# Kernel tuning notes

Hardware: AMD Instinct MI355X
Metric: run time of the kernel (lower is better)

Reference implementation:

```python
import jax, jax.numpy as jnp
import numpy as np

H = 16       # num_heads
D = 64       # head_dim
MBL = 2048   # max_bias_length


def setup_inputs() -> dict:
    key = jax.random.key(0)
    ks = jax.random.split(key, 7)
    B, L, E = 1, 2048, 1024
    s = E ** -0.5  # keep activations O(1)
    return {
        "x": jax.random.normal(ks[0], (B, L, E), jnp.float32),
        "Wq": jax.random.normal(ks[1], (E, E), jnp.float32) * s,
        "Wk": jax.random.normal(ks[2], (E, E), jnp.float32) * s,
        "Wv": jax.random.normal(ks[3], (E, E), jnp.float32) * s,
        "Wo": jax.random.normal(ks[4], (E, E), jnp.float32) * s,
        "bias": jax.random.normal(ks[5], (H, MBL), jnp.float32) * 0.001,
        "tau": jnp.full((H,), -1.0, jnp.float32),
    }


def reference(x, Wq, Wk, Wv, Wo, bias, tau):
    B, L, E = x.shape
    # projections (nn.Linear: y = x @ W.T), split into heads -> [B, H, L, D]
    q = (x @ Wq.T).reshape(B, L, H, D).transpose(0, 2, 1, 3)
    k = (x @ Wk.T).reshape(B, L, H, D).transpose(0, 2, 1, 3)
    v = (x @ Wv.T).reshape(B, L, H, D).transpose(0, 2, 1, 3)

    scale = D ** -0.5
    scores = jnp.einsum("bhqd,bhkd->bhqk", q, k) * scale  # [B,H,L,L]

    pos = jnp.arange(L)
    dist = pos[:, None] - pos[None, :]                     # [L,L] q - k
    dist_clamped = jnp.clip(dist, 0, MBL - 1)
    in_window = (dist >= 0) & (dist < MBL)
    bias_matrix = bias[:, dist_clamped] * in_window.astype(scores.dtype)  # [H,L,L]
    scores = scores + bias_matrix[None]

    causal = dist >= 0
    scores = jnp.where(causal[None, None], scores, -jnp.inf)
    attn = jax.nn.softmax(scores, axis=-1)                 # [B,H,L,L]

    # elastic-softmax correction: relu(attn + tau_h / row_index)
    idx = jnp.arange(1, L + 1, dtype=attn.dtype)           # 1..L per query row
    tau_term = tau[None, :, None, None] / idx[None, None, :, None]
    attn = jax.nn.relu(attn + tau_term)

    out = jnp.einsum("bhqk,bhkd->bhqd", attn, v)           # [B,H,L,D]
    out = out.transpose(0, 2, 1, 3).reshape(B, L, H * D)
    return out @ Wo.T
```

## Files before the change

### kernel.cpp

```cpp
#include <hip/hip_runtime.h>
#include <stdint.h>


typedef unsigned short u16;
typedef __bf16 bf16x8 __attribute__((ext_vector_type(8)));
typedef float f32x4 __attribute__((ext_vector_type(4)));

__device__ __forceinline__ void gl_lds16(const void* g, void* l) {
  __builtin_amdgcn_global_load_lds((const __attribute__((address_space(1))) void*)g,
                                   (__attribute__((address_space(3))) void*)l, 16, 0, 0);
}
__device__ __forceinline__ u16 f2b(float x) {
  return __builtin_bit_cast(u16, (__bf16)x);
}

__global__ __launch_bounds__(256) void conv_all(
    const float* __restrict__ x, const float* __restrict__ wq, const float* __restrict__ wk,
    const float* __restrict__ wv, const float* __restrict__ wo,
    u16* __restrict__ xb, u16* __restrict__ wqb, u16* __restrict__ wkb,
    u16* __restrict__ wvb, u16* __restrict__ wob) {
  int i4 = blockIdx.x * 256 + threadIdx.x;
  const float* s; u16* d; int off;
  if (i4 < 524288)       { s = x;  d = xb;  off = i4; }
  else if (i4 < 786432)  { s = wq; d = wqb; off = i4 - 524288; }
  else if (i4 < 1048576) { s = wk; d = wkb; off = i4 - 786432; }
  else if (i4 < 1310720) { s = wv; d = wvb; off = i4 - 1048576; }
  else                   { s = wo; d = wob; off = i4 - 1310720; }
  float4 v = reinterpret_cast<const float4*>(s)[off];
  ushort4 o;
  o.x = f2b(v.x); o.y = f2b(v.y); o.z = f2b(v.z); o.w = f2b(v.w);
  reinterpret_cast<ushort4*>(d)[off] = o;
}

template <int MT>
__device__ __forceinline__ void gemm_core(const u16* __restrict__ A, const u16* __restrict__ B,
                                          int m0, int n0, u16* As, u16* Bs,
                                          f32x4 (&acc)[MT / 32][4], int w, int l) {
  int lr = l & 15, lg = l >> 4;
  int wr = w >> 1, wc = w & 1;
  for (int k0 = 0; k0 < 1024; k0 += 32) {
    __syncthreads();
#pragma unroll
    for (int j = 0; j < MT / 64; ++j) {
      int flat = j * 256 + w * 64 + l;
      int row = flat >> 2, c = flat & 3;
      int cs = c ^ (row & 3);
      gl_lds16(A + (size_t)(m0 + row) * 1024 + k0 + cs * 8, As + (j * 256 + w * 64) * 8);
    }
#pragma unroll
    for (int j = 0; j < 2; ++j) {
      int flat = j * 256 + w * 64 + l;
      int row = flat >> 2, c = flat & 3;
      int cs = c ^ (row & 3);
      gl_lds16(B + (size_t)(n0 + row) * 1024 + k0 + cs * 8, Bs + (j * 256 + w * 64) * 8);
    }
    __syncthreads();
    bf16x8 af[MT / 32], bfr[4];
#pragma unroll
    for (int mi = 0; mi < MT / 32; ++mi) {
      int row = wr * (MT / 2) + mi * 16 + lr;
      af[mi] = *reinterpret_cast<const bf16x8*>(
          reinterpret_cast<const char*>(As) + row * 64 + ((lg * 16) ^ ((row & 3) << 4)));
    }
#pragma unroll
    for (int ni = 0; ni < 4; ++ni) {
      int row = wc * 64 + ni * 16 + lr;
      bfr[ni] = *reinterpret_cast<const bf16x8*>(
          reinterpret_cast<const char*>(Bs) + row * 64 + ((lg * 16) ^ ((row & 3) << 4)));
    }
#pragma unroll
    for (int mi = 0; mi < MT / 32; ++mi)
#pragma unroll
      for (int ni = 0; ni < 4; ++ni)
        acc[mi][ni] = __builtin_amdgcn_mfma_f32_16x16x32_bf16(af[mi], bfr[ni], acc[mi][ni], 0, 0, 0);
  }
}

__global__ __launch_bounds__(256) void qkv_gemm(
    const u16* __restrict__ xb, const u16* __restrict__ wqb, const u16* __restrict__ wkb,
    const u16* __restrict__ wvb, u16* __restrict__ Qb, u16* __restrict__ Kb, u16* __restrict__ Vtb) {
  __shared__ __align__(16) u16 As[64 * 32];
  __shared__ __align__(16) u16 Bs[128 * 32];
  int tid = threadIdx.x, w = tid >> 6, l = tid & 63;
  int lr = l & 15, lg = l >> 4;
  int wr = w >> 1, wc = w & 1;
  int mat = blockIdx.y >> 3;
  int m0 = blockIdx.x * 64, n0 = (blockIdx.y & 7) * 128;
  const u16* B = (mat == 0) ? wqb : (mat == 1) ? wkb : wvb;
  const f32x4 fz = {0.f, 0.f, 0.f, 0.f};
  f32x4 acc[2][4];
#pragma unroll
  for (int i = 0; i < 2; ++i)
#pragma unroll
    for (int j = 0; j < 4; ++j) acc[i][j] = fz;
  gemm_core<64>(xb, B, m0, n0, As, Bs, acc, w, l);
  if (mat < 2) {
    u16* O = (mat == 0) ? Qb : Kb;
    float sc = (mat == 0) ? 0.125f : 1.0f;
#pragma unroll
    for (int mi = 0; mi < 2; ++mi)
#pragma unroll
      for (int ni = 0; ni < 4; ++ni)
#pragma unroll
        for (int r = 0; r < 4; ++r) {
          int m = m0 + wr * 32 + mi * 16 + lg * 4 + r;
          int n = n0 + wc * 64 + ni * 16 + lr;
          O[(size_t)m * 1024 + n] = f2b(acc[mi][ni][r] * sc);
        }
  } else {
#pragma unroll
    for (int mi = 0; mi < 2; ++mi)
#pragma unroll
      for (int ni = 0; ni < 4; ++ni) {
        int n = n0 + wc * 64 + ni * 16 + lr;
        int m = m0 + wr * 32 + mi * 16 + lg * 4;
        ushort4 o;
        o.x = f2b(acc[mi][ni][0]); o.y = f2b(acc[mi][ni][1]);
        o.z = f2b(acc[mi][ni][2]); o.w = f2b(acc[mi][ni][3]);
        *reinterpret_cast<ushort4*>(Vtb + (size_t)n * 2048 + m) = o;
      }
  }
}

__global__ __launch_bounds__(256) void wo_gemm(const u16* __restrict__ Ab, const u16* __restrict__ Wb,
                                               float* __restrict__ out) {
  __shared__ __align__(16) u16 As[64 * 32];
  __shared__ __align__(16) u16 Bs[128 * 32];
  int tid = threadIdx.x, w = tid >> 6, l = tid & 63;
  int lr = l & 15, lg = l >> 4;
  int wr = w >> 1, wc = w & 1;
  int m0 = blockIdx.x * 64, n0 = blockIdx.y * 128;
  const f32x4 fz = {0.f, 0.f, 0.f, 0.f};
  f32x4 acc[2][4];
#pragma unroll
  for (int i = 0; i < 2; ++i)
#pragma unroll
    for (int j = 0; j < 4; ++j) acc[i][j] = fz;
  gemm_core<64>(Ab, Wb, m0, n0, As, Bs, acc, w, l);
#pragma unroll
  for (int mi = 0; mi < 2; ++mi)
#pragma unroll
    for (int ni = 0; ni < 4; ++ni)
#pragma unroll
      for (int r = 0; r < 4; ++r) {
        int m = m0 + wr * 32 + mi * 16 + lg * 4 + r;
        int n = n0 + wc * 64 + ni * 16 + lr;
        out[(size_t)m * 1024 + n] = acc[mi][ni][r];
      }
}

__global__ __launch_bounds__(512, 4) void attn_kernel(
    const u16* __restrict__ Qg, const u16* __restrict__ Kg, const u16* __restrict__ Vtg,
    const float* __restrict__ bias, const float* __restrict__ tau, u16* __restrict__ AO) {
  __shared__ __align__(16) float bias_s[2048];
  __shared__ __align__(16) u16 P_s[8][2][16 * 32];
  __shared__ float Zbuf[8][16];
  __shared__ __align__(16) float obuf[4][64][16];
  int bx = blockIdx.x, by = blockIdx.y;
  int qt = (by & 8) ? (31 - bx) : bx;
  int h = by;
  int tid = threadIdx.x, w = tid >> 6, l = tid & 63;
  int lr = l & 15, lg = l >> 4;
  int wq = w & 3, par = w >> 2;
  int qrow0 = qt * 64 + wq * 16;
  reinterpret_cast<float4*>(bias_s)[tid] =
      reinterpret_cast<const float4*>(bias + (size_t)h * 2048)[tid];
  float tauh = tau[h];
  const f32x4 fz = {0.f, 0.f, 0.f, 0.f};
  bf16x8 qf[2];
#pragma unroll
  for (int f = 0; f < 2; ++f)
    qf[f] = *reinterpret_cast<const bf16x8*>(Qg + (size_t)(qrow0 + lr) * 1024 + h * 64 + f * 32 + lg * 8);
  int qi_[4];
  float Z_r[4];
#pragma unroll
  for (int r = 0; r < 4; ++r) { qi_[r] = qrow0 + lg * 4 + r; Z_r[r] = 0.f; }
  int nkt = qt + 1;
  __syncthreads();

  for (int kt = par; kt < nkt; kt += 2) {
    int k0 = kt * 64;
    bf16x8 kb[4][2];
#pragma unroll
    for (int g = 0; g < 4; ++g)
#pragma unroll
      for (int f = 0; f < 2; ++f)
        kb[g][f] = *reinterpret_cast<const bf16x8*>(
            Kg + (size_t)(k0 + g * 16 + lr) * 1024 + h * 64 + f * 32 + lg * 8);
    f32x4 s[4];
#pragma unroll
    for (int g = 0; g < 4; ++g) {
      s[g] = fz;
#pragma unroll
      for (int f = 0; f < 2; ++f)
        s[g] = __builtin_amdgcn_mfma_f32_16x16x32_bf16(qf[f], kb[g][f], s[g], 0, 0, 0);
    }
#pragma unroll
    for (int g = 0; g < 4; ++g)
#pragma unroll
      for (int r = 0; r < 4; ++r) {
        int dist = qi_[r] - (k0 + g * 16 + lr);
        float e = __expf(s[g][r] + bias_s[dist < 0 ? 0 : dist]);
        Z_r[r] += (dist >= 0) ? e : 0.f;
      }
  }
#pragma unroll
  for (int r = 0; r < 4; ++r) {
    float z = Z_r[r];
    z += __shfl_xor(z, 1); z += __shfl_xor(z, 2);
    z += __shfl_xor(z, 4); z += __shfl_xor(z, 8);
    Z_r[r] = z;
    if (lr == 0) Zbuf[w][lg * 4 + r] = z;
  }
  __syncthreads();
  float invZ[4], cr[4];
#pragma unroll
  for (int r = 0; r < 4; ++r) {
    float z = Z_r[r] + Zbuf[w ^ 4][lg * 4 + r];
    invZ[r] = 1.f / z;
    cr[r] = tauh / (float)(qi_[r] + 1);
  }
  f32x4 oacc[4];
#pragma unroll
  for (int nf = 0; nf < 4; ++nf) oacc[nf] = fz;

  for (int kt = par; kt < nkt; kt += 2) {
    int k0 = kt * 64;
    bf16x8 kb[4][2];
#pragma unroll
    for (int g = 0; g < 4; ++g)
#pragma unroll
      for (int f = 0; f < 2; ++f)
        kb[g][f] = *reinterpret_cast<const bf16x8*>(
            Kg + (size_t)(k0 + g * 16 + lr) * 1024 + h * 64 + f * 32 + lg * 8);
    bf16x8 vb[4][2];
#pragma unroll
    for (int nf = 0; nf < 4; ++nf)
#pragma unroll
      for (int kk = 0; kk < 2; ++kk)
        vb[nf][kk] = *reinterpret_cast<const bf16x8*>(
            Vtg + (size_t)(h * 64 + nf * 16 + lr) * 2048 + k0 + kk * 32 + lg * 8);
    f32x4 s[4];
#pragma unroll
    for (int g = 0; g < 4; ++g) {
      s[g] = fz;
#pragma unroll
      for (int f = 0; f < 2; ++f)
        s[g] = __builtin_amdgcn_mfma_f32_16x16x32_bf16(qf[f], kb[g][f], s[g], 0, 0, 0);
    }
#pragma unroll
    for (int g = 0; g < 4; ++g)
#pragma unroll
      for (int r = 0; r < 4; ++r) {
        int dist = qi_[r] - (k0 + g * 16 + lr);
        float e = __expf(s[g][r] + bias_s[dist < 0 ? 0 : dist]);
        float a = fmaxf(__builtin_fmaf(e, invZ[r], cr[r]), 0.f);
        a = (dist >= 0) ? a : 0.f;
        int row = lg * 4 + r;
        int col32 = (g & 1) * 16 + lr;
        P_s[w][g >> 1][row * 32 + (col32 ^ ((row & 3) << 3))] = f2b(a);
      }
    bf16x8 pa[2];
#pragma unroll
    for (int kk = 0; kk < 2; ++kk)
      pa[kk] = *reinterpret_cast<const bf16x8*>(&P_s[w][kk][lr * 32 + ((lg * 8) ^ ((lr & 3) << 3))]);
#pragma unroll
    for (int nf = 0; nf < 4; ++nf)
#pragma unroll
      for (int kk = 0; kk < 2; ++kk)
        oacc[nf] = __builtin_amdgcn_mfma_f32_16x16x32_bf16(pa[kk], vb[nf][kk], oacc[nf], 0, 0, 0);
  }
  if (par == 1) {
#pragma unroll
    for (int nf = 0; nf < 4; ++nf)
      *reinterpret_cast<f32x4*>(&obuf[wq][l][nf * 4]) = oacc[nf];
  }
  __syncthreads();
  if (par == 0) {
#pragma unroll
    for (int nf = 0; nf < 4; ++nf) {
      oacc[nf] += *reinterpret_cast<const f32x4*>(&obuf[wq][l][nf * 4]);
#pragma unroll
      for (int r = 0; r < 4; ++r)
        AO[(size_t)(qrow0 + lg * 4 + r) * 1024 + h * 64 + nf * 16 + lr] = f2b(oacc[nf][r]);
    }
  }
}

extern "C" void kernel_launch(void* const* d_in, const int* in_sizes, int n_in,
                              void* d_out, int out_size, void* d_ws, size_t ws_size,
                              hipStream_t stream) {
  (void)in_sizes; (void)n_in; (void)out_size; (void)ws_size;
  const float* x    = (const float*)d_in[0];
  const float* Wq   = (const float*)d_in[1];
  const float* Wk   = (const float*)d_in[2];
  const float* Wv   = (const float*)d_in[3];
  const float* Wo   = (const float*)d_in[4];
  const float* bias = (const float*)d_in[5];
  const float* tau  = (const float*)d_in[6];
  float* out = (float*)d_out;

  char* ws = (char*)d_ws;
  u16* xb  = (u16*)ws; ws += (size_t)2048 * 1024 * 2;
  u16* wqb = (u16*)ws; ws += (size_t)1024 * 1024 * 2;
  u16* wkb = (u16*)ws; ws += (size_t)1024 * 1024 * 2;
  u16* wvb = (u16*)ws; ws += (size_t)1024 * 1024 * 2;
  u16* wob = (u16*)ws; ws += (size_t)1024 * 1024 * 2;
  u16* Qb  = (u16*)ws; ws += (size_t)2048 * 1024 * 2;
  u16* Kb  = (u16*)ws; ws += (size_t)2048 * 1024 * 2;
  u16* Vtb = (u16*)ws; ws += (size_t)1024 * 2048 * 2;
  u16* AO  = (u16*)ws; ws += (size_t)2048 * 1024 * 2;

  conv_all<<<6144, 256, 0, stream>>>(x, Wq, Wk, Wv, Wo, xb, wqb, wkb, wvb, wob);
  qkv_gemm<<<dim3(32, 24), 256, 0, stream>>>(xb, wqb, wkb, wvb, Qb, Kb, Vtb);
  attn_kernel<<<dim3(32, 16), 512, 0, stream>>>(Qb, Kb, Vtb, bias, tau, AO);
  wo_gemm<<<dim3(32, 8), 256, 0, stream>>>(AO, wob, out);
}
```

Baseline: 212.2 us.

## Split attention key tiles four ways and use base-2 exp with padded mask bias

The attention block grows from 512 to 1024 threads, so each query tile's key loop is split across four wave groups instead of two. Their partial row sums and outputs are combined through a two-step tree reduction that reuses the P_s shared buffer. The softmax now uses raw v_exp_f32: log2(e) is folded into the Q scale and the bias, and the bias table gets 64 leading -3e38 entries so masked positions exponentiate to zero without per-element branches. This cuts serial loop length and VALU work per element, at the cost of extra syncs and heavier LDS use per block, which may limit occupancy.

```diff
diff --git a/kernel.cpp b/kernel.cpp
--- a/kernel.cpp
+++ b/kernel.cpp
@@ -12,6 +12,11 @@
 }
 __device__ __forceinline__ u16 f2b(float x) {
   return __builtin_bit_cast(u16, (__bf16)x);
+}
+__device__ __forceinline__ float ex2(float x) {
+  float r;
+  asm("v_exp_f32 %0, %1" : "=v"(r) : "v"(x));
+  return r;
 }
 
 __global__ __launch_bounds__(256) void conv_all(
@@ -96,7 +101,7 @@
   gemm_core<64>(xb, B, m0, n0, As, Bs, acc, w, l);
   if (mat < 2) {
     u16* O = (mat == 0) ? Qb : Kb;
-    float sc = (mat == 0) ? 0.125f : 1.0f;
+    float sc = (mat == 0) ? 0.18033688f : 1.0f;
 #pragma unroll
     for (int mi = 0; mi < 2; ++mi)
 #pragma unroll
@@ -149,13 +154,12 @@
       }
 }
 
-__global__ __launch_bounds__(512, 4) void attn_kernel(
+__global__ __launch_bounds__(1024, 8) void attn_kernel(
     const u16* __restrict__ Qg, const u16* __restrict__ Kg, const u16* __restrict__ Vtg,
     const float* __restrict__ bias, const float* __restrict__ tau, u16* __restrict__ AO) {
-  __shared__ __align__(16) float bias_s[2048];
-  __shared__ __align__(16) u16 P_s[8][2][16 * 32];
-  __shared__ float Zbuf[8][16];
-  __shared__ __align__(16) float obuf[4][64][16];
+  __shared__ __align__(16) float bias_s[2112];
+  __shared__ __align__(16) u16 P_s[16][2][16 * 32];
+  __shared__ float Zbuf[16][16];
   int bx = blockIdx.x, by = blockIdx.y;
   int qt = (by & 8) ? (31 - bx) : bx;
   int h = by;
@@ -163,8 +167,8 @@
   int lr = l & 15, lg = l >> 4;
   int wq = w & 3, par = w >> 2;
   int qrow0 = qt * 64 + wq * 16;
-  reinterpret_cast<float4*>(bias_s)[tid] =
-      reinterpret_cast<const float4*>(bias + (size_t)h * 2048)[tid];
+  for (int i = tid; i < 2112; i += 1024)
+    bias_s[i] = (i < 64) ? -3.0e38f : bias[(size_t)h * 2048 + (i - 64)] * 1.44269504f;
   float tauh = tau[h];
   const f32x4 fz = {0.f, 0.f, 0.f, 0.f};
   bf16x8 qf[2];
@@ -178,7 +182,7 @@
   int nkt = qt + 1;
   __syncthreads();
 
-  for (int kt = par; kt < nkt; kt += 2) {
+  for (int kt = par; kt < nkt; kt += 4) {
     int k0 = kt * 64;
     bf16x8 kb[4][2];
 #pragma unroll
@@ -199,9 +203,8 @@
     for (int g = 0; g < 4; ++g)
 #pragma unroll
       for (int r = 0; r < 4; ++r) {
-        int dist = qi_[r] - (k0 + g * 16 + lr);
-        float e = __expf(s[g][r] + bias_s[dist < 0 ? 0 : dist]);
-        Z_r[r] += (dist >= 0) ? e : 0.f;
+        int ind = qi_[r] + 64 - (k0 + g * 16 + lr);
+        Z_r[r] += ex2(s[g][r] + bias_s[ind]);
       }
   }
 #pragma unroll
@@ -209,14 +212,14 @@
     float z = Z_r[r];
     z += __shfl_xor(z, 1); z += __shfl_xor(z, 2);
     z += __shfl_xor(z, 4); z += __shfl_xor(z, 8);
-    Z_r[r] = z;
     if (lr == 0) Zbuf[w][lg * 4 + r] = z;
   }
   __syncthreads();
   float invZ[4], cr[4];
 #pragma unroll
   for (int r = 0; r < 4; ++r) {
-    float z = Z_r[r] + Zbuf[w ^ 4][lg * 4 + r];
+    float z = Zbuf[wq][lg * 4 + r] + Zbuf[4 + wq][lg * 4 + r] +
+              Zbuf[8 + wq][lg * 4 + r] + Zbuf[12 + wq][lg * 4 + r];
     invZ[r] = 1.f / z;
     cr[r] = tauh / (float)(qi_[r] + 1);
   }
@@ -224,7 +227,7 @@
 #pragma unroll
   for (int nf = 0; nf < 4; ++nf) oacc[nf] = fz;
 
-  for (int kt = par; kt < nkt; kt += 2) {
+  for (int kt = par; kt < nkt; kt += 4) {
     int k0 = kt * 64;
     bf16x8 kb[4][2];
 #pragma unroll
@@ -252,10 +255,9 @@
     for (int g = 0; g < 4; ++g)
 #pragma unroll
       for (int r = 0; r < 4; ++r) {
-        int dist = qi_[r] - (k0 + g * 16 + lr);
-        float e = __expf(s[g][r] + bias_s[dist < 0 ? 0 : dist]);
+        int ind = qi_[r] + 64 - (k0 + g * 16 + lr);
+        float e = ex2(s[g][r] + bias_s[ind]);
         float a = fmaxf(__builtin_fmaf(e, invZ[r], cr[r]), 0.f);
-        a = (dist >= 0) ? a : 0.f;
         int row = lg * 4 + r;
         int col32 = (g & 1) * 16 + lr;
         P_s[w][g >> 1][row * 32 + (col32 ^ ((row & 3) << 3))] = f2b(a);
@@ -270,16 +272,32 @@
       for (int kk = 0; kk < 2; ++kk)
         oacc[nf] = __builtin_amdgcn_mfma_f32_16x16x32_bf16(pa[kk], vb[nf][kk], oacc[nf], 0, 0, 0);
   }
-  if (par == 1) {
-#pragma unroll
-    for (int nf = 0; nf < 4; ++nf)
-      *reinterpret_cast<f32x4*>(&obuf[wq][l][nf * 4]) = oacc[nf];
+
+  float* ob = reinterpret_cast<float*>(&P_s[0][0][0]);
+  float* slot0 = ob + ((size_t)(0 * 4 + wq) * 64 + l) * 16;
+  float* slot1 = ob + ((size_t)(1 * 4 + wq) * 64 + l) * 16;
+  __syncthreads();
+  if (par & 1) {
+    float* d = (par >> 1) ? slot1 : slot0;
+#pragma unroll
+    for (int nf = 0; nf < 4; ++nf) *reinterpret_cast<f32x4*>(d + nf * 4) = oacc[nf];
+  }
+  __syncthreads();
+  if (!(par & 1)) {
+    const float* sp = (par >> 1) ? slot1 : slot0;
+#pragma unroll
+    for (int nf = 0; nf < 4; ++nf) oacc[nf] += *reinterpret_cast<const f32x4*>(sp + nf * 4);
+  }
+  __syncthreads();
+  if (par == 2) {
+#pragma unroll
+    for (int nf = 0; nf < 4; ++nf) *reinterpret_cast<f32x4*>(slot0 + nf * 4) = oacc[nf];
   }
   __syncthreads();
   if (par == 0) {
 #pragma unroll
     for (int nf = 0; nf < 4; ++nf) {
-      oacc[nf] += *reinterpret_cast<const f32x4*>(&obuf[wq][l][nf * 4]);
+      oacc[nf] += *reinterpret_cast<const f32x4*>(slot0 + nf * 4);
 #pragma unroll
       for (int r = 0; r < 4; ++r)
         AO[(size_t)(qrow0 + lg * 4 + r) * 1024 + h * 64 + nf * 16 + lr] = f2b(oacc[nf][r]);
@@ -313,6 +331,6 @@
 
   conv_all<<<6144, 256, 0, stream>>>(x, Wq, Wk, Wv, Wo, xb, wqb, wkb, wvb, wob);
   qkv_gemm<<<dim3(32, 24), 256, 0, stream>>>(xb, wqb, wkb, wvb, Qb, Kb, Vtb);
-  attn_kernel<<<dim3(32, 16), 512, 0, stream>>>(Qb, Kb, Vtb, bias, tau, AO);
+  attn_kernel<<<dim3(32, 16), 1024, 0, stream>>>(Qb, Kb, Vtb, bias, tau, AO);
   wo_gemm<<<dim3(32, 8), 256, 0, stream>>>(AO, wob, out);
 }
```

Result: slower. 236.8 us (+11.6%).
